# Kernel tuning notes

Hardware: AMD Instinct MI355X
Metric: run time of the kernel (lower is better)

Reference implementation:

```python
import jax, jax.numpy as jnp
import numpy as np

SHAPES = ((92, 160), (46, 80), (23, 40), (12, 20))  # multi-scale (H, W) per level
B, NQ, C, M, P = 8, 900, 256, 8, 4
L = len(SHAPES)
D = C // M          # head dim = 32
S = sum(h * w for h, w in SHAPES)  # 19560 flattened keys
NC = 10
FFN = 1024


def setup_inputs() -> dict:
    key = jax.random.key(0)
    ks = jax.random.split(key, 16)
    f = lambda k, sh, s=0.02: jax.random.normal(k, sh, dtype=jnp.float32) * s
    return dict(
        query=jax.random.normal(ks[0], (B, NQ, C), dtype=jnp.float32),
        value=jax.random.normal(ks[1], (B, S, C), dtype=jnp.float32),
        ref_points=jax.random.uniform(ks[2], (B, NQ, 2), dtype=jnp.float32),
        w_value=f(ks[3], (C, C)), b_value=jnp.zeros((C,), jnp.float32),
        w_off=f(ks[4], (C, M * L * P * 2)), b_off=f(ks[5], (M * L * P * 2,), 0.5),
        w_attn=f(ks[6], (C, M * L * P)), b_attn=jnp.zeros((M * L * P,), jnp.float32),
        w_out=f(ks[7], (C, C)), b_out=jnp.zeros((C,), jnp.float32),
        ln1_w=jnp.ones((C,), jnp.float32), ln1_b=jnp.zeros((C,), jnp.float32),
        w_ffn1=f(ks[8], (C, FFN)), b_ffn1=jnp.zeros((FFN,), jnp.float32),
        w_ffn2=f(ks[9], (FFN, C)), b_ffn2=jnp.zeros((C,), jnp.float32),
        ln2_w=jnp.ones((C,), jnp.float32), ln2_b=jnp.zeros((C,), jnp.float32),
        w_cls=f(ks[10], (C, NC)), b_cls=jnp.zeros((NC,), jnp.float32),
    )


def _ln(x, w, b, eps=1e-6):
    u = x.mean(-1, keepdims=True)
    s = ((x - u) ** 2).mean(-1, keepdims=True)
    return (x - u) * jax.lax.rsqrt(s + eps) * w + b


def _sample_level(v_l, loc, Hl, Wl):
    # v_l: [B, Hl*Wl, M, D] level features; loc: [B, NQ, M, P, 2] normalized sampling locations.
    # Bilinear interpolation with zero padding (grid_sample align_corners=False convention).
    x = loc[..., 0] * Wl - 0.5
    y = loc[..., 1] * Hl - 0.5
    x0 = jnp.floor(x)
    y0 = jnp.floor(y)
    lx, ly = x - x0, y - y0
    vt = jnp.transpose(v_l, (0, 2, 1, 3))  # [B, M, S_l, D]

    def gather(xi, yi):
        valid = ((xi >= 0) & (xi < Wl) & (yi >= 0) & (yi < Hl)).astype(v_l.dtype)
        idx = (jnp.clip(yi, 0, Hl - 1) * Wl + jnp.clip(xi, 0, Wl - 1)).astype(jnp.int32)
        idx = jnp.transpose(idx, (0, 2, 1, 3)).reshape(B, M, NQ * P)
        g = jnp.take_along_axis(vt, idx[..., None], axis=2).reshape(B, M, NQ, P, D)
        return g * jnp.transpose(valid, (0, 2, 1, 3))[..., None]

    x0i, y0i = x0.astype(jnp.int32), y0.astype(jnp.int32)
    g00 = gather(x0i, y0i)
    g01 = gather(x0i + 1, y0i)
    g10 = gather(x0i, y0i + 1)
    g11 = gather(x0i + 1, y0i + 1)
    wx = jnp.transpose(lx, (0, 2, 1, 3))[..., None]
    wy = jnp.transpose(ly, (0, 2, 1, 3))[..., None]
    return g00 * (1 - wx) * (1 - wy) + g01 * wx * (1 - wy) + g10 * (1 - wx) * wy + g11 * wx * wy


def reference(query, value, ref_points, w_value, b_value, w_off, b_off, w_attn, b_attn,
              w_out, b_out, ln1_w, ln1_b, w_ffn1, b_ffn1, w_ffn2, b_ffn2, ln2_w, ln2_b,
              w_cls, b_cls):
    v = (value @ w_value + b_value).reshape(B, S, M, D)
    off = (query @ w_off + b_off).reshape(B, NQ, M, L, P, 2)
    attn = jax.nn.softmax((query @ w_attn + b_attn).reshape(B, NQ, M, L * P), axis=-1)
    attn = attn.reshape(B, NQ, M, L, P)
    norm = jnp.asarray([[w, h] for h, w in SHAPES], dtype=query.dtype)  # [L, 2] (W, H)
    loc = ref_points[:, :, None, None, None, :] + off / norm[None, None, None, :, None, :]

    out = jnp.zeros((B, M, NQ, D), dtype=query.dtype)
    start = 0
    for l, (Hl, Wl) in enumerate(SHAPES):
        v_l = jax.lax.dynamic_slice_in_dim(v, start, Hl * Wl, axis=1)
        samp = _sample_level(v_l, loc[:, :, :, l], Hl, Wl)          # [B, M, NQ, P, D]
        a = jnp.transpose(attn[:, :, :, l], (0, 2, 1, 3))[..., None]  # [B, M, NQ, P, 1]
        out = out + (samp * a).sum(3)
        start += Hl * Wl

    feat = jnp.transpose(out, (0, 2, 1, 3)).reshape(B, NQ, C) @ w_out + b_out
    x = _ln(query + feat, ln1_w, ln1_b)
    h = jax.nn.relu(x @ w_ffn1 + b_ffn1) @ w_ffn2 + b_ffn2
    x = _ln(x + h, ln2_w, ln2_b)
    return x @ w_cls + b_cls
```

## Files before the change

kernel.cpp:

```cpp
#include <hip/hip_runtime.h>
#include <cstddef>
#include <cstdint>

#define B_    8
#define NQ_   900
#define C_    256
#define M_    8
#define P_    4
#define L_    4
#define D_    32
#define S_    19560
#define NC_   10
#define FFN_  1024
#define RQ_   (B_ * NQ_)
#define RV_   (B_ * S_)


typedef __attribute__((ext_vector_type(8))) short bf8_t;
typedef __attribute__((ext_vector_type(4))) float f4_t;

__device__ __forceinline__ unsigned short f2bf(float x) {
    union { float f; unsigned u; } v; v.f = x;
    unsigned r = v.u + 0x7FFF + ((v.u >> 16) & 1);
    return (unsigned short)(r >> 16);
}

__global__ __launch_bounds__(256) void prep_weights(
    const float* __restrict__ w_value, const float* __restrict__ w_off,
    const float* __restrict__ w_attn,  const float* __restrict__ w_out,
    const float* __restrict__ w_ffn1,  const float* __restrict__ w_ffn2,
    short* __restrict__ WvT, short* __restrict__ WoaT, short* __restrict__ WoutT,
    short* __restrict__ Wf1T, short* __restrict__ Wf2T)
{
    const int mat = blockIdx.z;
    int K, N; const float* src; short* dst;
    switch (mat) {
        case 0: K = 256;  N = 256;  src = w_value; dst = WvT;  break;
        case 1: K = 256;  N = 384;  src = nullptr; dst = WoaT; break;
        case 2: K = 256;  N = 256;  src = w_out;   dst = WoutT; break;
        case 3: K = 256;  N = 1024; src = w_ffn1;  dst = Wf1T; break;
        default:K = 1024; N = 256;  src = w_ffn2;  dst = Wf2T; break;
    }
    const int ntn = N >> 6;
    const int kt = blockIdx.x / ntn, nt = blockIdx.x % ntn;
    if (kt >= (K >> 6)) return;

    __shared__ float t[64][65];
    const int tx = threadIdx.x & 63;
    const int ty = threadIdx.x >> 6;
#pragma unroll
    for (int i = 0; i < 64; i += 4) {
        const int k = kt * 64 + i + ty;
        const int n = nt * 64 + tx;
        float v;
        if (mat == 1) v = (n < 256) ? w_off[(size_t)k * 256 + n]
                                    : w_attn[(size_t)k * 128 + (n - 256)];
        else          v = src[(size_t)k * N + n];
        t[i + ty][tx] = v;
    }
    __syncthreads();
#pragma unroll
    for (int i = 0; i < 64; i += 4) {
        const int n = nt * 64 + i + ty;
        const int k = kt * 64 + tx;
        dst[(size_t)n * K + k] = (short)f2bf(t[tx][i + ty]);
    }
}

__global__ __launch_bounds__(384) void prep_bias(
    const float* __restrict__ b_off, const float* __restrict__ b_attn,
    float* __restrict__ bias_cat)
{
    const int t = threadIdx.x;
    bias_cat[t] = (t < 256) ? b_off[t] : b_attn[t - 256];
}

template <int MODE>
__global__ __launch_bounds__(256) void gemm_mfma(
    const float* __restrict__ A, const short* __restrict__ WT,
    const float* __restrict__ bias, const float* __restrict__ res,
    float* __restrict__ out, int R, int N, int K)
{
    __shared__ __align__(16) short As[128 * 64];
    __shared__ __align__(16) short Bs[128 * 64];

    const int tid  = threadIdx.x;
    const int lane = tid & 63;
    const int wave = tid >> 6;
    const int wr   = wave >> 1;
    const int wc   = wave & 1;
    const int g    = lane >> 4;
    const int fr   = lane & 15;

    const int row0 = blockIdx.x * 128;
    const int col0 = blockIdx.y * 128;

    f4_t acc[4][4] = {};

    for (int k0 = 0; k0 < K; k0 += 64) {
#pragma unroll
        for (int it = 0; it < 4; ++it) {
            const int unit = it * 256 + tid;
            const int r    = unit >> 3;
            const int ku   = unit & 7;
            float va[8] = {0.f, 0.f, 0.f, 0.f, 0.f, 0.f, 0.f, 0.f};
            const int grow = row0 + r;
            if (grow < R) {
                const float4 p0 = *(const float4*)(A + (size_t)grow * K + k0 + ku * 8);
                const float4 p1 = *(const float4*)(A + (size_t)grow * K + k0 + ku * 8 + 4);
                va[0] = p0.x; va[1] = p0.y; va[2] = p0.z; va[3] = p0.w;
                va[4] = p1.x; va[5] = p1.y; va[6] = p1.z; va[7] = p1.w;
            }
            bf8_t pk;
#pragma unroll
            for (int j = 0; j < 8; ++j) pk[j] = (short)f2bf(va[j]);
            const int u = ku ^ (r & 7);
            *(bf8_t*)&As[r * 64 + u * 8] = pk;
        }
#pragma unroll
        for (int it = 0; it < 4; ++it) {
            const int unit = it * 256 + tid;
            const int n    = unit >> 3;
            const int ku   = unit & 7;
            const int u    = ku ^ (n & 7);
            const int4 w = *(const int4*)(WT + (size_t)(col0 + n) * K + k0 + ku * 8);
            *(int4*)&Bs[n * 64 + u * 8] = w;
        }
        __syncthreads();

#pragma unroll
        for (int c = 0; c < 2; ++c) {
            bf8_t a[4], b[4];
#pragma unroll
            for (int i = 0; i < 4; ++i) {
                const int ar = wr * 64 + i * 16 + fr;
                const int au = (c * 4 + g) ^ (ar & 7);
                a[i] = *(const bf8_t*)&As[ar * 64 + au * 8];
                const int br = wc * 64 + i * 16 + fr;
                const int bu = (c * 4 + g) ^ (br & 7);
                b[i] = *(const bf8_t*)&Bs[br * 64 + bu * 8];
            }
#pragma unroll
            for (int i = 0; i < 4; ++i)
#pragma unroll
                for (int j = 0; j < 4; ++j)
                    acc[i][j] = __builtin_amdgcn_mfma_f32_16x16x32_bf16(
                        a[i], b[j], acc[i][j], 0, 0, 0);
        }
        __syncthreads();
    }

#pragma unroll
    for (int j = 0; j < 4; ++j) {
        const int col = col0 + wc * 64 + j * 16 + fr;
        const float bcol = bias[col];
#pragma unroll
        for (int i = 0; i < 4; ++i) {
#pragma unroll
            for (int r = 0; r < 4; ++r) {
                const int row = row0 + wr * 64 + i * 16 + g * 4 + r;
                if (row >= R) continue;
                float vv = acc[i][j][r] + bcol;
                if (MODE == 1) {
                    const int b = row / S_;
                    const int s = row - b * S_;
                    const int m = col >> 5;
                    const int d = col & 31;
                    out[(((size_t)(b * M_ + m)) * S_ + s) * D_ + d] = vv;
                } else if (MODE == 2) {
                    out[(size_t)row * N + col] = fmaxf(vv, 0.f);
                } else if (MODE == 3) {
                    out[(size_t)row * N + col] = vv + res[(size_t)row * N + col];
                } else {
                    out[(size_t)row * N + col] = vv;
                }
            }
        }
    }
}

__global__ __launch_bounds__(128) void softmax_loc_kernel(
    const float* __restrict__ oa, const float* __restrict__ ref,
    float* __restrict__ loc, float* __restrict__ attn)
{
    const int row = blockIdx.x;
    const int t   = threadIdx.x;
    const float Wtab[L_] = {160.f, 80.f, 40.f, 20.f};
    const float Htab[L_] = {92.f, 46.f, 23.f, 12.f};

    float vlog = oa[(size_t)row * 384 + 256 + t];
    float mx = vlog;
#pragma unroll
    for (int o = 8; o >= 1; o >>= 1) mx = fmaxf(mx, __shfl_xor(mx, o, 64));
    const float e = __expf(vlog - mx);
    float sm = e;
#pragma unroll
    for (int o = 8; o >= 1; o >>= 1) sm += __shfl_xor(sm, o, 64);
    attn[(size_t)row * 128 + t] = e / sm;

    const int m = t >> 4, l = (t >> 2) & 3, p = t & 3;
    const float rx = ref[(size_t)row * 2 + 0];
    const float ry = ref[(size_t)row * 2 + 1];
    const int oi = m * 32 + l * 8 + p * 2;
    loc[(size_t)row * 256 + oi + 0] = rx * Wtab[l] + oa[(size_t)row * 384 + oi + 0] - 0.5f;
    loc[(size_t)row * 256 + oi + 1] = ry * Htab[l] + oa[(size_t)row * 384 + oi + 1] - 0.5f;
}

__global__ __launch_bounds__(256) void sample_kernel(
    const float* __restrict__ v, const float* __restrict__ loc,
    const float* __restrict__ attn, float* __restrict__ outf)
{
    const int row = blockIdx.x;
    const int b   = row / NQ_;
    const int t   = threadIdx.x;
    const int m   = t >> 5;
    const int d   = t & 31;

    __shared__ float sloc[256];
    __shared__ float satt[128];
    sloc[t] = loc[(size_t)row * 256 + t];
    if (t < 128) satt[t] = attn[(size_t)row * 128 + t];
    __syncthreads();

    const int Wtab[L_] = {160, 80, 40, 20};
    const int Htab[L_] = {92, 46, 23, 12};
    const int Stab[L_] = {0, 14720, 18400, 19320};

    const float* vb = v + ((size_t)(b * M_ + m)) * S_ * D_ + d;
    float acc = 0.f;

#pragma unroll
    for (int l = 0; l < L_; ++l) {
        const int Wl = Wtab[l], Hl = Htab[l], st = Stab[l];
#pragma unroll
        for (int p = 0; p < P_; ++p) {
            const float x = sloc[m * 32 + l * 8 + p * 2 + 0];
            const float y = sloc[m * 32 + l * 8 + p * 2 + 1];
            const float a = satt[m * 16 + l * 4 + p];
            const float xf = floorf(x), yf = floorf(y);
            const int x0 = (int)xf, y0 = (int)yf;
            const float lx = x - xf, ly = y - yf;
            const float w00 = (1.f - lx) * (1.f - ly);
            const float w01 = lx * (1.f - ly);
            const float w10 = (1.f - lx) * ly;
            const float w11 = lx * ly;
            const bool xv0 = (x0 >= 0) && (x0 < Wl);
            const bool xv1 = (x0 + 1 >= 0) && (x0 + 1 < Wl);
            const bool yv0 = (y0 >= 0) && (y0 < Hl);
            const bool yv1 = (y0 + 1 >= 0) && (y0 + 1 < Hl);
            float s00 = 0.f, s01 = 0.f, s10 = 0.f, s11 = 0.f;
            if (xv0 && yv0) s00 = vb[(size_t)(st + y0 * Wl + x0) * D_];
            if (xv1 && yv0) s01 = vb[(size_t)(st + y0 * Wl + x0 + 1) * D_];
            if (xv0 && yv1) s10 = vb[(size_t)(st + (y0 + 1) * Wl + x0) * D_];
            if (xv1 && yv1) s11 = vb[(size_t)(st + (y0 + 1) * Wl + x0 + 1) * D_];
            acc += a * (w00 * s00 + w01 * s01 + w10 * s10 + w11 * s11);
        }
    }
    outf[(size_t)row * 256 + m * 32 + d] = acc;
}

__global__ __launch_bounds__(64) void ln_kernel(
    const float* __restrict__ in, const float* __restrict__ w,
    const float* __restrict__ bp, float* __restrict__ out)
{
    const int row  = blockIdx.x;
    const int lane = threadIdx.x;
    const float4 x = ((const float4*)(in + (size_t)row * C_))[lane];
    float s = x.x + x.y + x.z + x.w;
#pragma unroll
    for (int o = 32; o >= 1; o >>= 1) s += __shfl_xor(s, o, 64);
    const float mean = s * (1.f / C_);
    const float d0 = x.x - mean, d1 = x.y - mean, d2 = x.z - mean, d3 = x.w - mean;
    float ss = d0 * d0 + d1 * d1 + d2 * d2 + d3 * d3;
#pragma unroll
    for (int o = 32; o >= 1; o >>= 1) ss += __shfl_xor(ss, o, 64);
    const float r = rsqrtf(ss * (1.f / C_) + 1e-6f);
    const float4 wv = ((const float4*)w)[lane];
    const float4 bv = ((const float4*)bp)[lane];
    float4 o4;
    o4.x = d0 * r * wv.x + bv.x;
    o4.y = d1 * r * wv.y + bv.y;
    o4.z = d2 * r * wv.z + bv.z;
    o4.w = d3 * r * wv.w + bv.w;
    ((float4*)(out + (size_t)row * C_))[lane] = o4;
}

__global__ __launch_bounds__(64) void cls_kernel(
    const float* __restrict__ x, const float* __restrict__ w,
    const float* __restrict__ bias, float* __restrict__ out)
{
    const int row  = blockIdx.x;
    const int lane = threadIdx.x;
    float acc[NC_] = {};
#pragma unroll
    for (int j = 0; j < 4; ++j) {
        const int k = lane + j * 64;
        const float xk = x[(size_t)row * C_ + k];
        const float* wr = w + (size_t)k * NC_;
#pragma unroll
        for (int n = 0; n < NC_; ++n) acc[n] += xk * wr[n];
    }
#pragma unroll
    for (int n = 0; n < NC_; ++n) {
        float s = acc[n];
#pragma unroll
        for (int o = 32; o >= 1; o >>= 1) s += __shfl_xor(s, o, 64);
        if (lane == n) out[(size_t)row * NC_ + n] = s + bias[n];
    }
}

extern "C" void kernel_launch(void* const* d_in, const int* in_sizes, int n_in,
                              void* d_out, int out_size, void* d_ws, size_t ws_size,
                              hipStream_t stream)
{
    const float* query   = (const float*)d_in[0];
    const float* value   = (const float*)d_in[1];
    const float* refp    = (const float*)d_in[2];
    const float* w_value = (const float*)d_in[3];
    const float* b_value = (const float*)d_in[4];
    const float* w_off   = (const float*)d_in[5];
    const float* b_off   = (const float*)d_in[6];
    const float* w_attn  = (const float*)d_in[7];
    const float* b_attn  = (const float*)d_in[8];
    const float* w_out   = (const float*)d_in[9];
    const float* b_out   = (const float*)d_in[10];
    const float* ln1w    = (const float*)d_in[11];
    const float* ln1b    = (const float*)d_in[12];
    const float* w_ffn1  = (const float*)d_in[13];
    const float* b_ffn1  = (const float*)d_in[14];
    const float* w_ffn2  = (const float*)d_in[15];
    const float* b_ffn2  = (const float*)d_in[16];
    const float* ln2w    = (const float*)d_in[17];
    const float* ln2b    = (const float*)d_in[18];
    const float* w_cls   = (const float*)d_in[19];
    const float* b_cls   = (const float*)d_in[20];

    short* WvT   = (short*)d_ws;
    short* WoaT  = WvT  + 65536;
    short* WoutT = WoaT + 98304;
    short* Wf1T  = WoutT + 65536;
    short* Wf2T  = Wf1T + 262144;
    float* bias_cat = (float*)(Wf2T + 262144);
    float* v    = bias_cat + 384;
    float* oa   = v    + (size_t)RV_ * C_;
    float* loc  = oa   + (size_t)RQ_ * 384;
    float* attn = loc  + (size_t)RQ_ * 256;
    float* feat = attn + (size_t)RQ_ * 128;
    float* tmp  = feat + (size_t)RQ_ * 256;
    float* h    = tmp  + (size_t)RQ_ * 256;
    float* x2   = h    + (size_t)RQ_ * FFN_;

    prep_weights<<<dim3(64, 1, 5), 256, 0, stream>>>(
        w_value, w_off, w_attn, w_out, w_ffn1, w_ffn2,
        WvT, WoaT, WoutT, Wf1T, Wf2T);
    prep_bias<<<1, 384, 0, stream>>>(b_off, b_attn, bias_cat);

    gemm_mfma<1><<<dim3((RV_ + 127) / 128, 2), 256, 0, stream>>>(
        value, WvT, b_value, nullptr, v, RV_, 256, 256);

    gemm_mfma<0><<<dim3((RQ_ + 127) / 128, 3), 256, 0, stream>>>(
        query, WoaT, bias_cat, nullptr, oa, RQ_, 384, 256);

    softmax_loc_kernel<<<RQ_, 128, 0, stream>>>(oa, refp, loc, attn);

    sample_kernel<<<RQ_, 256, 0, stream>>>(v, loc, attn, feat);

    gemm_mfma<3><<<dim3((RQ_ + 127) / 128, 2), 256, 0, stream>>>(
        feat, WoutT, b_out, query, tmp, RQ_, 256, 256);

    ln_kernel<<<RQ_, 64, 0, stream>>>(tmp, ln1w, ln1b, feat);

    gemm_mfma<2><<<dim3((RQ_ + 127) / 128, 8), 256, 0, stream>>>(
        feat, Wf1T, b_ffn1, nullptr, h, RQ_, 1024, 256);

    gemm_mfma<3><<<dim3((RQ_ + 127) / 128, 2), 256, 0, stream>>>(
        h, Wf2T, b_ffn2, feat, tmp, RQ_, 256, 1024);

    ln_kernel<<<RQ_, 64, 0, stream>>>(tmp, ln2w, ln2b, x2);

    cls_kernel<<<RQ_, 64, 0, stream>>>(x2, w_cls, b_cls, (float*)d_out);
}
```

Measured before the change: 610.3 us.

## Store projected values as bf16, prefetch GEMM tiles, use smaller row tiles

The value projection now writes bf16 through an LDS-staged, vectorized epilogue, and the sampling kernel reads and widens bf16 values. This halves the size of the largest intermediate tensor and its gather traffic. The GEMM also prefetches the next K tile into registers while MFMAs run on the current one. The query-side GEMMs use 64-row tiles to launch more blocks for the small row count. The cost is lower precision in the sampled values and more register pressure.

```diff
diff --git a/kernel.cpp b/kernel.cpp
--- a/kernel.cpp
+++ b/kernel.cpp
@@ -15,14 +15,17 @@
 #define RQ_   (B_ * NQ_)
 #define RV_   (B_ * S_)
 
-
 typedef __attribute__((ext_vector_type(8))) short bf8_t;
 typedef __attribute__((ext_vector_type(4))) float f4_t;
+typedef unsigned short ushort_t;
 
 __device__ __forceinline__ unsigned short f2bf(float x) {
     union { float f; unsigned u; } v; v.f = x;
     unsigned r = v.u + 0x7FFF + ((v.u >> 16) & 1);
     return (unsigned short)(r >> 16);
+}
+__device__ __forceinline__ float bfu2f(unsigned short u) {
+    union { unsigned u; float f; } v; v.u = ((unsigned)u) << 16; return v.f;
 }
 
 __global__ __launch_bounds__(256) void prep_weights(
@@ -75,14 +78,20 @@
     bias_cat[t] = (t < 256) ? b_off[t] : b_attn[t - 256];
 }
 
-template <int MODE>
+template <int MODE, int BM>
 __global__ __launch_bounds__(256) void gemm_mfma(
     const float* __restrict__ A, const short* __restrict__ WT,
     const float* __restrict__ bias, const float* __restrict__ res,
     float* __restrict__ out, int R, int N, int K)
 {
-    __shared__ __align__(16) short As[128 * 64];
-    __shared__ __align__(16) short Bs[128 * 64];
+    constexpr int NI  = BM / 32;
+    constexpr int AIT = BM * 8 / 256;
+    constexpr int ASB = BM * 128;
+    constexpr int SMEM_BYTES = (MODE == 1) ? (128 * 136 * 2) : (ASB + 16384);
+
+    __shared__ __align__(16) char smem[SMEM_BYTES];
+    short* As = (short*)smem;
+    short* Bs = (short*)(smem + ASB);
 
     const int tid  = threadIdx.x;
     const int lane = tid & 63;
@@ -92,87 +101,134 @@
     const int g    = lane >> 4;
     const int fr   = lane & 15;
 
-    const int row0 = blockIdx.x * 128;
+    const int row0 = blockIdx.x * BM;
     const int col0 = blockIdx.y * 128;
 
-    f4_t acc[4][4] = {};
-
+    const int r_base = tid >> 3;
+    const int ku     = tid & 7;
+
+    float4 rA[AIT][2];
+#pragma unroll
+    for (int it = 0; it < AIT; ++it) {
+        rA[it][0] = make_float4(0.f, 0.f, 0.f, 0.f);
+        rA[it][1] = make_float4(0.f, 0.f, 0.f, 0.f);
+    }
+    int4 rB[4];
+
+    f4_t acc[NI][4] = {};
+
+    auto LOAD = [&](int k0) {
+#pragma unroll
+        for (int it = 0; it < AIT; ++it) {
+            const int grow = row0 + it * 32 + r_base;
+            if (grow < R) {
+                rA[it][0] = *(const float4*)(A + (size_t)grow * K + k0 + ku * 8);
+                rA[it][1] = *(const float4*)(A + (size_t)grow * K + k0 + ku * 8 + 4);
+            }
+        }
+#pragma unroll
+        for (int it = 0; it < 4; ++it) {
+            const int n = it * 32 + r_base;
+            rB[it] = *(const int4*)(WT + (size_t)(col0 + n) * K + k0 + ku * 8);
+        }
+    };
+    auto WRITE = [&]() {
+#pragma unroll
+        for (int it = 0; it < AIT; ++it) {
+            const int r = it * 32 + r_base;
+            const float va[8] = {rA[it][0].x, rA[it][0].y, rA[it][0].z, rA[it][0].w,
+                                 rA[it][1].x, rA[it][1].y, rA[it][1].z, rA[it][1].w};
+            bf8_t pk;
+#pragma unroll
+            for (int j = 0; j < 8; ++j) pk[j] = (short)f2bf(va[j]);
+            *(bf8_t*)&As[r * 64 + (ku ^ (r & 7)) * 8] = pk;
+        }
+#pragma unroll
+        for (int it = 0; it < 4; ++it) {
+            const int n = it * 32 + r_base;
+            *(int4*)&Bs[n * 64 + (ku ^ (n & 7)) * 8] = rB[it];
+        }
+    };
+
+    LOAD(0);
     for (int k0 = 0; k0 < K; k0 += 64) {
-#pragma unroll
-        for (int it = 0; it < 4; ++it) {
-            const int unit = it * 256 + tid;
-            const int r    = unit >> 3;
-            const int ku   = unit & 7;
-            float va[8] = {0.f, 0.f, 0.f, 0.f, 0.f, 0.f, 0.f, 0.f};
-            const int grow = row0 + r;
-            if (grow < R) {
-                const float4 p0 = *(const float4*)(A + (size_t)grow * K + k0 + ku * 8);
-                const float4 p1 = *(const float4*)(A + (size_t)grow * K + k0 + ku * 8 + 4);
-                va[0] = p0.x; va[1] = p0.y; va[2] = p0.z; va[3] = p0.w;
-                va[4] = p1.x; va[5] = p1.y; va[6] = p1.z; va[7] = p1.w;
+        WRITE();
+        __syncthreads();
+        if (k0 + 64 < K) LOAD(k0 + 64);
+#pragma unroll
+        for (int c = 0; c < 2; ++c) {
+            bf8_t fa[NI], fb[4];
+#pragma unroll
+            for (int i = 0; i < NI; ++i) {
+                const int ar = wr * (BM / 2) + i * 16 + fr;
+                fa[i] = *(const bf8_t*)&As[ar * 64 + ((c * 4 + g) ^ (ar & 7)) * 8];
             }
-            bf8_t pk;
-#pragma unroll
-            for (int j = 0; j < 8; ++j) pk[j] = (short)f2bf(va[j]);
-            const int u = ku ^ (r & 7);
-            *(bf8_t*)&As[r * 64 + u * 8] = pk;
-        }
-#pragma unroll
-        for (int it = 0; it < 4; ++it) {
-            const int unit = it * 256 + tid;
-            const int n    = unit >> 3;
-            const int ku   = unit & 7;
-            const int u    = ku ^ (n & 7);
-            const int4 w = *(const int4*)(WT + (size_t)(col0 + n) * K + k0 + ku * 8);
-            *(int4*)&Bs[n * 64 + u * 8] = w;
-        }
-        __syncthreads();
-
-#pragma unroll
-        for (int c = 0; c < 2; ++c) {
-            bf8_t a[4], b[4];
-#pragma unroll
-            for (int i = 0; i < 4; ++i) {
-                const int ar = wr * 64 + i * 16 + fr;
-                const int au = (c * 4 + g) ^ (ar & 7);
-                a[i] = *(const bf8_t*)&As[ar * 64 + au * 8];
-                const int br = wc * 64 + i * 16 + fr;
-                const int bu = (c * 4 + g) ^ (br & 7);
-                b[i] = *(const bf8_t*)&Bs[br * 64 + bu * 8];
+#pragma unroll
+            for (int j = 0; j < 4; ++j) {
+                const int br = wc * 64 + j * 16 + fr;
+                fb[j] = *(const bf8_t*)&Bs[br * 64 + ((c * 4 + g) ^ (br & 7)) * 8];
             }
 #pragma unroll
-            for (int i = 0; i < 4; ++i)
+            for (int i = 0; i < NI; ++i)
 #pragma unroll
                 for (int j = 0; j < 4; ++j)
                     acc[i][j] = __builtin_amdgcn_mfma_f32_16x16x32_bf16(
-                        a[i], b[j], acc[i][j], 0, 0, 0);
+                        fa[i], fb[j], acc[i][j], 0, 0, 0);
         }
         __syncthreads();
     }
 
-#pragma unroll
-    for (int j = 0; j < 4; ++j) {
-        const int col = col0 + wc * 64 + j * 16 + fr;
-        const float bcol = bias[col];
-#pragma unroll
-        for (int i = 0; i < 4; ++i) {
-#pragma unroll
-            for (int r = 0; r < 4; ++r) {
-                const int row = row0 + wr * 64 + i * 16 + g * 4 + r;
-                if (row >= R) continue;
-                float vv = acc[i][j][r] + bcol;
-                if (MODE == 1) {
-                    const int b = row / S_;
-                    const int s = row - b * S_;
-                    const int m = col >> 5;
-                    const int d = col & 31;
-                    out[(((size_t)(b * M_ + m)) * S_ + s) * D_ + d] = vv;
-                } else if (MODE == 2) {
-                    out[(size_t)row * N + col] = fmaxf(vv, 0.f);
-                } else if (MODE == 3) {
-                    out[(size_t)row * N + col] = vv + res[(size_t)row * N + col];
-                } else {
-                    out[(size_t)row * N + col] = vv;
+    if (MODE == 1) {
+        ushort_t* eps = (ushort_t*)smem;
+        ushort_t* outv = (ushort_t*)out;
+#pragma unroll
+        for (int j = 0; j < 4; ++j) {
+            const int col_l = wc * 64 + j * 16 + fr;
+            const float bcol = bias[col0 + col_l];
+#pragma unroll
+            for (int i = 0; i < NI; ++i)
+#pragma unroll
+                for (int r = 0; r < 4; ++r) {
+                    const int row_l = wr * 64 + i * 16 + g * 4 + r;
+                    eps[row_l * 136 + col_l] = f2bf(acc[i][j][r] + bcol);
+                }
+        }
+        __syncthreads();
+#pragma unroll
+        for (int u = 0; u < 8; ++u) {
+            const int unit = u * 256 + tid;
+            const int sl = unit >> 4;
+            const int cc = unit & 15;
+            const int grow = row0 + sl;
+            if (grow < R) {
+                const int b = grow / S_;
+                const int s = grow - b * S_;
+                const int col = col0 + cc * 8;
+                const int m = col >> 5;
+                const int d = col & 31;
+                const int4 w = *(const int4*)&eps[sl * 136 + cc * 8];
+                *(int4*)&outv[(((size_t)(b * M_ + m)) * S_ + s) * D_ + d] = w;
+            }
+        }
+    } else {
+#pragma unroll
+        for (int j = 0; j < 4; ++j) {
+            const int col = col0 + wc * 64 + j * 16 + fr;
+            const float bcol = bias[col];
+#pragma unroll
+            for (int i = 0; i < NI; ++i) {
+#pragma unroll
+                for (int r = 0; r < 4; ++r) {
+                    const int row = row0 + wr * (BM / 2) + i * 16 + g * 4 + r;
+                    if (row >= R) continue;
+                    float vv = acc[i][j][r] + bcol;
+                    if (MODE == 2) {
+                        out[(size_t)row * N + col] = fmaxf(vv, 0.f);
+                    } else if (MODE == 3) {
+                        out[(size_t)row * N + col] = vv + res[(size_t)row * N + col];
+                    } else {
+                        out[(size_t)row * N + col] = vv;
+                    }
                 }
             }
         }
@@ -207,7 +263,7 @@
 }
 
 __global__ __launch_bounds__(256) void sample_kernel(
-    const float* __restrict__ v, const float* __restrict__ loc,
+    const ushort_t* __restrict__ v, const float* __restrict__ loc,
     const float* __restrict__ attn, float* __restrict__ outf)
 {
     const int row = blockIdx.x;
@@ -226,7 +282,7 @@
     const int Htab[L_] = {92, 46, 23, 12};
     const int Stab[L_] = {0, 14720, 18400, 19320};
 
-    const float* vb = v + ((size_t)(b * M_ + m)) * S_ * D_ + d;
+    const ushort_t* vb = v + ((size_t)(b * M_ + m)) * S_ * D_ + d;
     float acc = 0.f;
 
 #pragma unroll
@@ -249,10 +305,10 @@
             const bool yv0 = (y0 >= 0) && (y0 < Hl);
             const bool yv1 = (y0 + 1 >= 0) && (y0 + 1 < Hl);
             float s00 = 0.f, s01 = 0.f, s10 = 0.f, s11 = 0.f;
-            if (xv0 && yv0) s00 = vb[(size_t)(st + y0 * Wl + x0) * D_];
-            if (xv1 && yv0) s01 = vb[(size_t)(st + y0 * Wl + x0 + 1) * D_];
-            if (xv0 && yv1) s10 = vb[(size_t)(st + (y0 + 1) * Wl + x0) * D_];
-            if (xv1 && yv1) s11 = vb[(size_t)(st + (y0 + 1) * Wl + x0 + 1) * D_];
+            if (xv0 && yv0) s00 = bfu2f(vb[(size_t)(st + y0 * Wl + x0) * D_]);
+            if (xv1 && yv0) s01 = bfu2f(vb[(size_t)(st + y0 * Wl + x0 + 1) * D_]);
+            if (xv0 && yv1) s10 = bfu2f(vb[(size_t)(st + (y0 + 1) * Wl + x0) * D_]);
+            if (xv1 && yv1) s11 = bfu2f(vb[(size_t)(st + (y0 + 1) * Wl + x0 + 1) * D_]);
             acc += a * (w00 * s00 + w01 * s01 + w10 * s10 + w11 * s11);
         }
     }
@@ -341,8 +397,8 @@
     short* Wf1T  = WoutT + 65536;
     short* Wf2T  = Wf1T + 262144;
     float* bias_cat = (float*)(Wf2T + 262144);
-    float* v    = bias_cat + 384;
-    float* oa   = v    + (size_t)RV_ * C_;
+    ushort_t* v = (ushort_t*)(bias_cat + 384);
+    float* oa   = (float*)(v + (size_t)RV_ * C_);
     float* loc  = oa   + (size_t)RQ_ * 384;
     float* attn = loc  + (size_t)RQ_ * 256;
     float* feat = attn + (size_t)RQ_ * 128;
@@ -355,25 +411,25 @@
         WvT, WoaT, WoutT, Wf1T, Wf2T);
     prep_bias<<<1, 384, 0, stream>>>(b_off, b_attn, bias_cat);
 
-    gemm_mfma<1><<<dim3((RV_ + 127) / 128, 2), 256, 0, stream>>>(
-        value, WvT, b_value, nullptr, v, RV_, 256, 256);
-
-    gemm_mfma<0><<<dim3((RQ_ + 127) / 128, 3), 256, 0, stream>>>(
+    gemm_mfma<1, 128><<<dim3((RV_ + 127) / 128, 2), 256, 0, stream>>>(
+        value, WvT, b_value, nullptr, (float*)v, RV_, 256, 256);
+
+    gemm_mfma<0, 64><<<dim3((RQ_ + 63) / 64, 3), 256, 0, stream>>>(
         query, WoaT, bias_cat, nullptr, oa, RQ_, 384, 256);
 
     softmax_loc_kernel<<<RQ_, 128, 0, stream>>>(oa, refp, loc, attn);
 
     sample_kernel<<<RQ_, 256, 0, stream>>>(v, loc, attn, feat);
 
-    gemm_mfma<3><<<dim3((RQ_ + 127) / 128, 2), 256, 0, stream>>>(
+    gemm_mfma<3, 64><<<dim3((RQ_ + 63) / 64, 2), 256, 0, stream>>>(
         feat, WoutT, b_out, query, tmp, RQ_, 256, 256);
 
     ln_kernel<<<RQ_, 64, 0, stream>>>(tmp, ln1w, ln1b, feat);
 
-    gemm_mfma<2><<<dim3((RQ_ + 127) / 128, 8), 256, 0, stream>>>(
+    gemm_mfma<2, 64><<<dim3((RQ_ + 63) / 64, 8), 256, 0, stream>>>(
         feat, Wf1T, b_ffn1, nullptr, h, RQ_, 1024, 256);
 
-    gemm_mfma<3><<<dim3((RQ_ + 127) / 128, 2), 256, 0, stream>>>(
+    gemm_mfma<3, 64><<<dim3((RQ_ + 63) / 64, 2), 256, 0, stream>>>(
         h, Wf2T, b_ffn2, feat, tmp, RQ_, 256, 1024);
 
     ln_kernel<<<RQ_, 64, 0, stream>>>(tmp, ln2w, ln2b, x2);
```

Result: slower. 661.0 us (+8.3%).
